# Kernel optimization log

Measured on AMD Instinct MI355X. Metric: run time of the kernel, lower is better.

The kernel has to match this reference:

```python
import jax, jax.numpy as jnp
import numpy as np

Z_WHAT = 64      # z_what latent size
DEC = 64         # decoded object patch size
IMG = 128        # output canvas size (ssd_config.DATA.SHAPE[0])
HID = 1024       # what-decoder hidden size
FEATURE_MAPS = [4, 2, 1]
BOXES_PER_LOC = [2, 2, 2]
B = 16


def build_indices():
    # Faithful port of Decoder.reconstruction_indices
    idx = []
    img_idx = last = 0
    for fm, bpl in zip(FEATURE_MAPS, BOXES_PER_LOC):
        for f in range(fm * fm):
            img_idx = last + f
            idx.append(np.full(bpl, img_idx, dtype=np.int32))
        last = img_idx + 1
    return np.concatenate(idx)


def setup_inputs() -> dict:
    key = jax.random.key(0)
    ks = jax.random.split(key, 6)
    idx = build_indices()
    N = idx.shape[0]            # 42 boxes
    NL = int(idx.max()) + 1     # 21 locations
    z_present = jax.random.randint(ks[4], (B, N, 1), 0, 2, jnp.int32)
    z_present = z_present.at[:, 0, 0].set(1)  # ensure >=1 present per image
    return {
        "z_what": jax.random.normal(ks[0], (B, NL, Z_WHAT), jnp.float32),
        "z_where": jax.random.uniform(ks[1], (B, N, 4), jnp.float32, 0.05, 0.95),
        "z_depth": jax.random.normal(ks[2], (B, NL, 1), jnp.float32),
        "w1": jax.random.normal(ks[3], (Z_WHAT, HID), jnp.float32) * 0.05,
        "b1": jnp.zeros((HID,), jnp.float32),
        "w2": jax.random.normal(ks[5], (HID, 3 * DEC * DEC), jnp.float32) * 0.05,
        "b2": jnp.zeros((3 * DEC * DEC,), jnp.float32),
        "z_present": z_present,
        "indices": jnp.asarray(idx),
    }


def _sample_one(img, px, py):
    # Bilinear grid-sample (zeros padding, align_corners=False) of one
    # [3,S,S] patch at pixel coords px, py of shape [H,W].
    S = img.shape[-1]
    x0 = jnp.floor(px)
    y0 = jnp.floor(py)
    wx = px - x0
    wy = py - y0
    x0i = x0.astype(jnp.int32)
    y0i = y0.astype(jnp.int32)

    def gather(xi, yi):
        valid = (xi >= 0) & (xi < S) & (yi >= 0) & (yi < S)
        v = img[:, jnp.clip(yi, 0, S - 1), jnp.clip(xi, 0, S - 1)]
        return v * valid[None].astype(img.dtype)

    return (gather(x0i, y0i) * ((1 - wx) * (1 - wy))[None]
            + gather(x0i + 1, y0i) * (wx * (1 - wy))[None]
            + gather(x0i, y0i + 1) * ((1 - wx) * wy)[None]
            + gather(x0i + 1, y0i + 1) * (wx * wy)[None])


def _forward(z_what, z_where, z_depth, w1, b1, w2, b2, z_present, indices):
    Bb, NL, D = z_what.shape
    N = indices.shape[0]
    # index_select: expand per-location latents to per-box
    zw = jnp.take(z_what, indices, axis=1)          # [B,N,D]
    zd = jnp.take(z_depth, indices, axis=1)[..., 0]  # [B,N]

    # WhatDecoder: MLP -> sigmoid -> [B*N,3,DEC,DEC] object patches
    h = jax.nn.relu(zw.reshape(-1, D) @ w1 + b1)
    dec = jax.nn.sigmoid(h @ w2 + b2).reshape(-1, 3, DEC, DEC)

    # WhereTransformer: place each patch into IMG x IMG canvas via
    # inverse-affine STN from z_where = (cx, cy, w, h) in [0,1].
    zwf = z_where.reshape(-1, 4)
    cx, cy, w, hh = zwf[:, 0], zwf[:, 1], zwf[:, 2], zwf[:, 3]
    t = (jnp.arange(IMG, dtype=z_what.dtype) + 0.5) / IMG * 2.0 - 1.0
    xt = t[None, :]  # [1,IMG]
    yt = t[:, None]  # [IMG,1]
    xs = (xt[None] - (2 * cx - 1)[:, None, None]) / jnp.maximum(w, 1e-6)[:, None, None]
    ys = (yt[None] - (2 * cy - 1)[:, None, None]) / jnp.maximum(hh, 1e-6)[:, None, None]
    px = ((xs + 1) * DEC - 1) / 2  # [B*N,IMG,IMG]
    py = ((ys + 1) * DEC - 1) / 2
    trans = jax.vmap(_sample_one)(dec, px, py).reshape(Bb, N, 3, IMG, IMG)

    # Masked softmax over depth == padded softmax with -inf starter in the
    # original: absent objects get exactly zero merge weight.
    masked = jnp.where(z_present[..., 0] == 1, zd, -jnp.inf)
    wgt = jax.nn.softmax(masked, axis=1)  # [B,N]
    return jnp.einsum('bn,bnchw->bchw', wgt, trans)


def reference(z_what, z_where, z_depth, w1, b1, w2, b2, z_present, indices):
    return _forward(z_what, z_where, z_depth, w1, b1, w2, b2, z_present, indices)
```

## Files before the change

### kernel.cpp

```cpp
#include <hip/hip_runtime.h>

#define B_    16
#define NL    21
#define NG    42
#define ZW    64
#define HID   1024
#define IMG   128
#define NOUT  12288
#define MROWS 336
#define MPAD  384

typedef __bf16 bf16x8 __attribute__((ext_vector_type(8)));
typedef float f32x4 __attribute__((ext_vector_type(4)));
typedef unsigned short ushort8v __attribute__((ext_vector_type(8)));
typedef unsigned short ushort4v __attribute__((ext_vector_type(4)));

static __device__ __forceinline__ unsigned short f2bf(float f) {
    union { float f; unsigned int u; } v; v.f = f;
    unsigned int r = v.u + 0x7fffu + ((v.u >> 16) & 1u);
    return (unsigned short)(r >> 16);
}

static __device__ __forceinline__ void gload_lds16(const void* g, void* l) {
    __builtin_amdgcn_global_load_lds(
        (const __attribute__((address_space(1))) void*)g,
        (__attribute__((address_space(3))) void*)l,
        16, 0, 0);
}

__global__ __launch_bounds__(256) void k0_w2_transpose(const float* __restrict__ w2,
                                                       unsigned short* __restrict__ w2t) {
    __shared__ float tile[64][65];
    const int nt = blockIdx.x;
    const int kt = blockIdx.y;
    const int t  = threadIdx.x;
    const int n0 = nt * 64, k0 = kt * 64;
    #pragma unroll
    for (int i = 0; i < 4; ++i) {
        int lin = i * 256 + t;
        int kr  = lin >> 4;
        int nc  = (lin & 15) << 2;
        float4 v = *reinterpret_cast<const float4*>(w2 + (size_t)(k0 + kr) * NOUT + n0 + nc);
        tile[kr][nc + 0] = v.x; tile[kr][nc + 1] = v.y;
        tile[kr][nc + 2] = v.z; tile[kr][nc + 3] = v.w;
    }
    __syncthreads();
    #pragma unroll
    for (int i = 0; i < 4; ++i) {
        int lin = i * 256 + t;
        int nc  = lin >> 4;
        int kc  = (lin & 15) << 2;
        ushort4v r;
        r.x = f2bf(tile[kc + 0][nc]);
        r.y = f2bf(tile[kc + 1][nc]);
        r.z = f2bf(tile[kc + 2][nc]);
        r.w = f2bf(tile[kc + 3][nc]);
        int kc_s = kc ^ ((nc & 7) << 3);
        *reinterpret_cast<ushort4v*>(w2t + (size_t)(n0 + nc) * HID + k0 + kc_s) = r;
    }
}

__global__ __launch_bounds__(256) void k1_h(const float* __restrict__ z_what,
                                            const float* __restrict__ w1,
                                            const float* __restrict__ b1,
                                            unsigned short* __restrict__ h) {
    const int r = blockIdx.x, t = threadIdx.x;
    const int sw = (r & 7) << 3;
    if (r >= MROWS) {
        #pragma unroll
        for (int i = 0; i < 4; ++i) {
            int k = t + i * 256;
            h[(size_t)r * HID + ((k & ~63) | ((k & 63) ^ sw))] = 0;
        }
        return;
    }
    __shared__ float zs[ZW];
    if (t < ZW) zs[t] = z_what[(size_t)r * ZW + t];
    __syncthreads();
    float acc[4];
    #pragma unroll
    for (int i = 0; i < 4; ++i) acc[i] = b1[t + i * 256];
    for (int k = 0; k < ZW; ++k) {
        float z = zs[k];
        const float* wr = w1 + (size_t)k * HID + t;
        acc[0] = fmaf(z, wr[0],   acc[0]);
        acc[1] = fmaf(z, wr[256], acc[1]);
        acc[2] = fmaf(z, wr[512], acc[2]);
        acc[3] = fmaf(z, wr[768], acc[3]);
    }
    #pragma unroll
    for (int i = 0; i < 4; ++i) {
        int k = t + i * 256;
        h[(size_t)r * HID + ((k & ~63) | ((k & 63) ^ sw))] =
            f2bf(acc[i] > 0.f ? acc[i] : 0.f);
    }
}

__global__ void k3_params(const float* __restrict__ z_where,
                          const float* __restrict__ z_depth,
                          const int* __restrict__ z_present,
                          const int* __restrict__ indices,
                          float* __restrict__ params) {
    const int b = blockIdx.x, t = threadIdx.x;
    const bool valid = t < NG;
    int idx  = valid ? indices[t] : 0;
    int pres = valid ? z_present[b * NG + t] : 0;
    float zd = z_depth[b * NL + idx];
    const bool on = valid && (pres == 1);
    float val = on ? zd : -__builtin_inff();
    float m = val;
    #pragma unroll
    for (int off = 32; off; off >>= 1) m = fmaxf(m, __shfl_xor(m, off));
    float e = on ? __expf(val - m) : 0.f;
    float s = e;
    #pragma unroll
    for (int off = 32; off; off >>= 1) s += __shfl_xor(s, off);
    if (valid) {
        float wn = e / s;
        const float* zw = z_where + (size_t)(b * NG + t) * 4;
        float cx = zw[0], cy = zw[1], ww = zw[2], hh = zw[3];
        float wm = fmaxf(ww, 1e-6f), hm = fmaxf(hh, 1e-6f);
        float Ax = 32.f / wm, Ay = 32.f / hm;
        float Bx = 31.5f - (2.f * cx - 1.f) * Ax;
        float By = 31.5f - (2.f * cy - 1.f) * Ay;
        float xlof = ((-1.f - Bx) / Ax + 1.f) * 64.f - 0.5f;
        float xhif = (( 64.f - Bx) / Ax + 1.f) * 64.f - 0.5f;
        float ylof = ((-1.f - By) / Ay + 1.f) * 64.f - 0.5f;
        float yhif = (( 64.f - By) / Ay + 1.f) * 64.f - 0.5f;
        int xlo = max(0,   (int)floorf(xlof));
        int xhi = min(128, (int)floorf(xhif) + 2);
        int ylo = max(0,   (int)floorf(ylof));
        int yhi = min(128, (int)floorf(yhif) + 2);
        float* p = params + (size_t)(b * NG + t) * 16;
        p[0] = wn; p[1] = Ax; p[2] = Bx; p[3] = Ay; p[4] = By;
        p[5] = __int_as_float(b * NL + idx);
        p[6] = __int_as_float(xlo); p[7] = __int_as_float(xhi);
        p[8] = __int_as_float(ylo); p[9] = __int_as_float(yhi);
    }
}

__global__ __launch_bounds__(256) void k2_gemm(const unsigned short* __restrict__ h,
                                               const unsigned short* __restrict__ w2t,
                                               const float* __restrict__ b2,
                                               float* __restrict__ dec) {
    __shared__ char smem[65536];
    const int t    = threadIdx.x;
    const int bn   = blockIdx.x;
    const int bm   = blockIdx.y;
    const int row0 = bm * 128, col0 = bn * 128;
    const int lane = t & 63, wid = t >> 6;
    const int wr = (wid >> 1) * 64, wc = (wid & 1) * 64;

    f32x4 acc[4][4];
    const f32x4 zero = {0.f, 0.f, 0.f, 0.f};
    #pragma unroll
    for (int m = 0; m < 4; ++m)
        #pragma unroll
        for (int n = 0; n < 4; ++n) acc[m][n] = zero;

    const char* hB = (const char*)h   + ((size_t)row0 << 11);
    const char* wB = (const char*)w2t + ((size_t)col0 << 11);

    #define STAGE(kt_, buf_)                                                        \
        do {                                                                        \
            int kby = (kt_) << 7;                                    \
            char* ldsA = smem + (buf_) * 32768;                                     \
            char* ldsB = ldsA + 16384;                                              \
            _Pragma("unroll")                                                       \
            for (int r_ = 0; r_ < 4; ++r_) {                                        \
                int ci  = r_ * 256 + t;                                             \
                int row = ci >> 3, kc = ci & 7;                                     \
                gload_lds16(hB + ((size_t)row << 11) + kby + (kc << 4),             \
                            ldsA + ci * 16);                                        \
                gload_lds16(wB + ((size_t)row << 11) + kby + (kc << 4),             \
                            ldsB + ci * 16);                                        \
            }                                                                       \
        } while (0)

    #define COMPUTE(buf_)                                                           \
        do {                                                                        \
            const char* Ab = smem + (buf_) * 32768;                                 \
            const char* Bb = Ab + 16384;                                            \
            _Pragma("unroll")                                                       \
            for (int ks = 0; ks < 2; ++ks) {                                        \
                int kb = ks * 64 + ((lane >> 4) << 4);                              \
                bf16x8 a[4], bb[4];                                                 \
                _Pragma("unroll")                                                   \
                for (int m = 0; m < 4; ++m) {                                       \
                    int row = wr + m * 16 + (lane & 15);                            \
                    a[m] = *reinterpret_cast<const bf16x8*>(                        \
                        Ab + row * 128 + (kb ^ ((row & 7) << 4)));                  \
                }                                                                   \
                _Pragma("unroll")                                                   \
                for (int n = 0; n < 4; ++n) {                                       \
                    int col = wc + n * 16 + (lane & 15);                            \
                    bb[n] = *reinterpret_cast<const bf16x8*>(                       \
                        Bb + col * 128 + (kb ^ ((col & 7) << 4)));                  \
                }                                                                   \
                _Pragma("unroll")                                                   \
                for (int m = 0; m < 4; ++m)                                         \
                    _Pragma("unroll")                                               \
                    for (int n = 0; n < 4; ++n)                                     \
                        acc[m][n] = __builtin_amdgcn_mfma_f32_16x16x32_bf16(        \
                            a[m], bb[n], acc[m][n], 0, 0, 0);                       \
            }                                                                       \
        } while (0)

    STAGE(0, 0);
    __syncthreads();
    int cur = 0;
    for (int kt = 1; kt < 16; ++kt) {
        STAGE(kt, cur ^ 1);
        COMPUTE(cur);
        __syncthreads();
        cur ^= 1;
    }
    COMPUTE(cur);

    const int rbase = row0 + wr + ((lane >> 4) << 2);
    const int cbase = col0 + wc + (lane & 15);
    #pragma unroll
    for (int n = 0; n < 4; ++n) {
        int col = cbase + n * 16;
        float bias = b2[col];
        #pragma unroll
        for (int m = 0; m < 4; ++m) {
            #pragma unroll
            for (int j = 0; j < 4; ++j) {
                int row = rbase + m * 16 + j;
                float v = acc[m][n][j] + bias;
                dec[(size_t)row * NOUT + col] = 1.f / (1.f + __expf(-v));
            }
        }
    }
    #undef STAGE
    #undef COMPUTE
}

__global__ __launch_bounds__(256) void k4_composite(const float* __restrict__ dec,
                                                    const float* __restrict__ params,
                                                    float* __restrict__ out) {
    __shared__ float Pc[NG * 6];
    __shared__ int s_cnt;
    const int b    = blockIdx.x >> 6;
    const int tile = blockIdx.x & 63;
    const int tx0 = (tile & 7) << 4, ty0 = (tile >> 3) << 4;
    const int t    = threadIdx.x;
    if (t < 64) {
        bool pass = false;
        float wn = 0.f, Ax = 0.f, Bx = 0.f, Ay = 0.f, By = 0.f, ridx = 0.f;
        if (t < NG) {
            const float* p = params + (size_t)(b * NG + t) * 16;
            wn = p[0];
            if (wn != 0.f) {
                int xlo = __float_as_int(p[6]), xhi = __float_as_int(p[7]);
                int ylo = __float_as_int(p[8]), yhi = __float_as_int(p[9]);
                if (xlo < tx0 + 16 && xhi > tx0 && ylo < ty0 + 16 && yhi > ty0) {
                    pass = true; Ax = p[1]; Bx = p[2]; Ay = p[3]; By = p[4]; ridx = p[5];
                }
            }
        }
        unsigned long long mask = __ballot(pass);
        if (pass) {
            int slot = __popcll(mask & ((1ull << t) - 1ull));
            float* q = Pc + slot * 6;
            q[0] = wn; q[1] = Ax; q[2] = Bx; q[3] = Ay; q[4] = By; q[5] = ridx;
        }
        if (t == 0) s_cnt = __popcll(mask);
    }
    __syncthreads();
    const int cnt = s_cnt;
    const int x = tx0 + (t & 15);
    const int y = ty0 + (t >> 4);
    const float xt = (x + 0.5f) * (1.f / 64.f) - 1.f;
    const float yt = (y + 0.5f) * (1.f / 64.f) - 1.f;
    float a0 = 0.f, a1 = 0.f, a2 = 0.f;
    for (int i = 0; i < cnt; ++i) {
        const float* q = Pc + i * 6;
        float wn = q[0];
        float px = fmaf(xt, q[1], q[2]);
        float py = fmaf(yt, q[3], q[4]);
        if (!(px > -1.f && px < 64.f && py > -1.f && py < 64.f)) continue;
        float x0f = floorf(px), y0f = floorf(py);
        float wx = px - x0f, wy = py - y0f;
        int x0 = (int)x0f, y0 = (int)y0f;
        int x1 = x0 + 1, y1 = y0 + 1;
        bool vx0 = x0 >= 0, vx1 = x1 < 64, vy0 = y0 >= 0, vy1 = y1 < 64;
        int ridx = __float_as_int(q[5]);
        const float* base = dec + (size_t)ridx * NOUT;
        float w00 = (1.f - wx) * (1.f - wy), w10 = wx * (1.f - wy);
        float w01 = (1.f - wx) * wy,         w11 = wx * wy;
        int o00 = y0 * 64 + x0, o10 = y0 * 64 + x1;
        int o01 = y1 * 64 + x0, o11 = y1 * 64 + x1;
        #pragma unroll
        for (int c = 0; c < 3; ++c) {
            const float* cb = base + c * 4096;
            float v00 = (vx0 && vy0) ? cb[o00] : 0.f;
            float v10 = (vx1 && vy0) ? cb[o10] : 0.f;
            float v01 = (vx0 && vy1) ? cb[o01] : 0.f;
            float v11 = (vx1 && vy1) ? cb[o11] : 0.f;
            float sv = v00 * w00 + v10 * w10 + v01 * w01 + v11 * w11;
            if      (c == 0) a0 = fmaf(wn, sv, a0);
            else if (c == 1) a1 = fmaf(wn, sv, a1);
            else             a2 = fmaf(wn, sv, a2);
        }
    }
    out[((size_t)(b * 3 + 0) * IMG + y) * IMG + x] = a0;
    out[((size_t)(b * 3 + 1) * IMG + y) * IMG + x] = a1;
    out[((size_t)(b * 3 + 2) * IMG + y) * IMG + x] = a2;
}

extern "C" void kernel_launch(void* const* d_in, const int* in_sizes, int n_in,
                              void* d_out, int out_size, void* d_ws, size_t ws_size,
                              hipStream_t stream) {
    const float* z_what   = (const float*)d_in[0];
    const float* z_where  = (const float*)d_in[1];
    const float* z_depth  = (const float*)d_in[2];
    const float* w1       = (const float*)d_in[3];
    const float* b1       = (const float*)d_in[4];
    const float* w2       = (const float*)d_in[5];
    const float* b2       = (const float*)d_in[6];
    const int*   z_present= (const int*)d_in[7];
    const int*   indices  = (const int*)d_in[8];
    float* out = (float*)d_out;

    char* ws = (char*)d_ws;
    unsigned short* w2t = (unsigned short*)ws;
    unsigned short* h   = (unsigned short*)(ws + 25165824);
    float*          dec = (float*)(ws + 25165824 + 786432);
    float*       params = (float*)(ws + 25165824 + 786432 + 18874368);

    hipLaunchKernelGGL(k0_w2_transpose, dim3(192, 16), dim3(256), 0, stream, w2, w2t);
    hipLaunchKernelGGL(k1_h,            dim3(MPAD),    dim3(256), 0, stream, z_what, w1, b1, h);
    hipLaunchKernelGGL(k3_params,       dim3(B_),      dim3(64),  0, stream, z_where, z_depth, z_present, indices, params);
    hipLaunchKernelGGL(k2_gemm,         dim3(96, 3),   dim3(256), 0, stream, h, w2t, b2, dec);
    hipLaunchKernelGGL(k4_composite,    dim3(1024),    dim3(256), 0, stream, dec, params, out);
}
```

Before: 145.3 us.

## Fuse all decoder stages into one cooperative persistent kernel with grid syncs

Replaces the five separate launches (transpose, hidden layer, params, GEMM, composite) with a single cooperative kernel of 256 persistent blocks that loops over tasks per phase and separates phases with grid-wide syncs. If cooperative launch fails, it falls back to three kernels, with the first three stages merged into one launch. The aim is to remove launch overhead and inter-kernel gaps. The cost is grid sync latency and a less even distribution, since the 288 GEMM tiles over 256 blocks create a tail wave.

```diff
diff --git a/kernel.cpp b/kernel.cpp
--- a/kernel.cpp
+++ b/kernel.cpp
@@ -1,4 +1,7 @@
 #include <hip/hip_runtime.h>
+#include <hip/hip_cooperative_groups.h>
+
+namespace cg = cooperative_groups;
 
 #define B_    16
 #define NL    21
@@ -9,10 +12,10 @@
 #define NOUT  12288
 #define MROWS 336
 #define MPAD  384
+#define CGRID 256
 
 typedef __bf16 bf16x8 __attribute__((ext_vector_type(8)));
 typedef float f32x4 __attribute__((ext_vector_type(4)));
-typedef unsigned short ushort8v __attribute__((ext_vector_type(8)));
 typedef unsigned short ushort4v __attribute__((ext_vector_type(4)));
 
 static __device__ __forceinline__ unsigned short f2bf(float f) {
@@ -28,19 +31,20 @@
         16, 0, 0);
 }
 
-__global__ __launch_bounds__(256) void k0_w2_transpose(const float* __restrict__ w2,
-                                                       unsigned short* __restrict__ w2t) {
-    __shared__ float tile[64][65];
-    const int nt = blockIdx.x;
-    const int kt = blockIdx.y;
-    const int t  = threadIdx.x;
-    const int n0 = nt * 64, k0 = kt * 64;
+
+static __device__ __forceinline__ void phaseA_tile(const float* __restrict__ w2,
+                                                   unsigned short* __restrict__ w2t,
+                                                   int task, int t, char* smem) {
+    float (*tile)[65] = reinterpret_cast<float (*)[65]>(smem);
+    const int nt = task % 192, kt = task / 192;
+    const int n0 = nt * 64,    k0 = kt * 64;
     #pragma unroll
     for (int i = 0; i < 4; ++i) {
         int lin = i * 256 + t;
         int kr  = lin >> 4;
         int nc  = (lin & 15) << 2;
-        float4 v = *reinterpret_cast<const float4*>(w2 + (size_t)(k0 + kr) * NOUT + n0 + nc);
+        float4 v = *reinterpret_cast<const float4*>(
+            w2 + (size_t)(k0 + kr) * NOUT + n0 + nc);
         tile[kr][nc + 0] = v.x; tile[kr][nc + 1] = v.y;
         tile[kr][nc + 2] = v.z; tile[kr][nc + 3] = v.w;
     }
@@ -56,15 +60,17 @@
         r.z = f2bf(tile[kc + 2][nc]);
         r.w = f2bf(tile[kc + 3][nc]);
         int kc_s = kc ^ ((nc & 7) << 3);
-        *reinterpret_cast<ushort4v*>(w2t + (size_t)(n0 + nc) * HID + k0 + kc_s) = r;
-    }
-}
-
-__global__ __launch_bounds__(256) void k1_h(const float* __restrict__ z_what,
-                                            const float* __restrict__ w1,
-                                            const float* __restrict__ b1,
-                                            unsigned short* __restrict__ h) {
-    const int r = blockIdx.x, t = threadIdx.x;
+        *reinterpret_cast<ushort4v*>(
+            w2t + (size_t)(n0 + nc) * HID + k0 + kc_s) = r;
+    }
+    __syncthreads();
+}
+
+static __device__ __forceinline__ void phaseB_row(const float* __restrict__ z_what,
+                                                  const float* __restrict__ w1,
+                                                  const float* __restrict__ b1,
+                                                  unsigned short* __restrict__ h,
+                                                  int r, int t, char* smem) {
     const int sw = (r & 7) << 3;
     if (r >= MROWS) {
         #pragma unroll
@@ -74,7 +80,7 @@
         }
         return;
     }
-    __shared__ float zs[ZW];
+    float* zs = reinterpret_cast<float*>(smem);
     if (t < ZW) zs[t] = z_what[(size_t)r * ZW + t];
     __syncthreads();
     float acc[4];
@@ -94,14 +100,16 @@
         h[(size_t)r * HID + ((k & ~63) | ((k & 63) ^ sw))] =
             f2bf(acc[i] > 0.f ? acc[i] : 0.f);
     }
-}
-
-__global__ void k3_params(const float* __restrict__ z_where,
-                          const float* __restrict__ z_depth,
-                          const int* __restrict__ z_present,
-                          const int* __restrict__ indices,
-                          float* __restrict__ params) {
-    const int b = blockIdx.x, t = threadIdx.x;
+    __syncthreads();
+}
+
+static __device__ __forceinline__ void phaseC_batch(const float* __restrict__ z_where,
+                                                    const float* __restrict__ z_depth,
+                                                    const int* __restrict__ z_present,
+                                                    const int* __restrict__ indices,
+                                                    float* __restrict__ params,
+                                                    int b, int t) {
+    if (t >= 64) return;
     const bool valid = t < NG;
     int idx  = valid ? indices[t] : 0;
     int pres = valid ? z_present[b * NG + t] : 0;
@@ -139,14 +147,13 @@
     }
 }
 
-__global__ __launch_bounds__(256) void k2_gemm(const unsigned short* __restrict__ h,
-                                               const unsigned short* __restrict__ w2t,
-                                               const float* __restrict__ b2,
-                                               float* __restrict__ dec) {
-    __shared__ char smem[65536];
-    const int t    = threadIdx.x;
-    const int bn   = blockIdx.x;
-    const int bm   = blockIdx.y;
+static __device__ __forceinline__ void phaseD_tile(const unsigned short* __restrict__ h,
+                                                   const unsigned short* __restrict__ w2t,
+                                                   const float* __restrict__ b2,
+                                                   float* __restrict__ dec,
+                                                   int task, int t, char* smem) {
+    const int bn   = task % 96;
+    const int bm   = task / 96;
     const int row0 = bm * 128, col0 = bn * 128;
     const int lane = t & 63, wid = t >> 6;
     const int wr = (wid >> 1) * 64, wc = (wid & 1) * 64;
@@ -161,49 +168,49 @@
     const char* hB = (const char*)h   + ((size_t)row0 << 11);
     const char* wB = (const char*)w2t + ((size_t)col0 << 11);
 
-    #define STAGE(kt_, buf_)                                                        \
-        do {                                                                        \
-            int kby = (kt_) << 7;                                    \
-            char* ldsA = smem + (buf_) * 32768;                                     \
-            char* ldsB = ldsA + 16384;                                              \
-            _Pragma("unroll")                                                       \
-            for (int r_ = 0; r_ < 4; ++r_) {                                        \
-                int ci  = r_ * 256 + t;                                             \
-                int row = ci >> 3, kc = ci & 7;                                     \
-                gload_lds16(hB + ((size_t)row << 11) + kby + (kc << 4),             \
-                            ldsA + ci * 16);                                        \
-                gload_lds16(wB + ((size_t)row << 11) + kby + (kc << 4),             \
-                            ldsB + ci * 16);                                        \
-            }                                                                       \
+    #define STAGE(kt_, buf_)                                                    \
+        do {                                                                    \
+            int kby = (kt_) << 7;                                               \
+            char* ldsA = smem + (buf_) * 32768;                                 \
+            char* ldsB = ldsA + 16384;                                          \
+            _Pragma("unroll")                                                   \
+            for (int r_ = 0; r_ < 4; ++r_) {                                    \
+                int ci  = r_ * 256 + t;                                         \
+                int row = ci >> 3, kc = ci & 7;                                 \
+                gload_lds16(hB + ((size_t)row << 11) + kby + (kc << 4),         \
+                            ldsA + ci * 16);                                    \
+                gload_lds16(wB + ((size_t)row << 11) + kby + (kc << 4),         \
+                            ldsB + ci * 16);                                    \
+            }                                                                   \
         } while (0)
 
-    #define COMPUTE(buf_)                                                           \
-        do {                                                                        \
-            const char* Ab = smem + (buf_) * 32768;                                 \
-            const char* Bb = Ab + 16384;                                            \
-            _Pragma("unroll")                                                       \
-            for (int ks = 0; ks < 2; ++ks) {                                        \
-                int kb = ks * 64 + ((lane >> 4) << 4);                              \
-                bf16x8 a[4], bb[4];                                                 \
-                _Pragma("unroll")                                                   \
-                for (int m = 0; m < 4; ++m) {                                       \
-                    int row = wr + m * 16 + (lane & 15);                            \
-                    a[m] = *reinterpret_cast<const bf16x8*>(                        \
-                        Ab + row * 128 + (kb ^ ((row & 7) << 4)));                  \
-                }                                                                   \
-                _Pragma("unroll")                                                   \
-                for (int n = 0; n < 4; ++n) {                                       \
-                    int col = wc + n * 16 + (lane & 15);                            \
-                    bb[n] = *reinterpret_cast<const bf16x8*>(                       \
-                        Bb + col * 128 + (kb ^ ((col & 7) << 4)));                  \
-                }                                                                   \
-                _Pragma("unroll")                                                   \
-                for (int m = 0; m < 4; ++m)                                         \
-                    _Pragma("unroll")                                               \
-                    for (int n = 0; n < 4; ++n)                                     \
-                        acc[m][n] = __builtin_amdgcn_mfma_f32_16x16x32_bf16(        \
-                            a[m], bb[n], acc[m][n], 0, 0, 0);                       \
-            }                                                                       \
+    #define COMPUTE(buf_)                                                       \
+        do {                                                                    \
+            const char* Ab = smem + (buf_) * 32768;                             \
+            const char* Bb = Ab + 16384;                                        \
+            _Pragma("unroll")                                                   \
+            for (int ks = 0; ks < 2; ++ks) {                                    \
+                int kb = ks * 64 + ((lane >> 4) << 4);                          \
+                bf16x8 a[4], bb[4];                                             \
+                _Pragma("unroll")                                               \
+                for (int m = 0; m < 4; ++m) {                                   \
+                    int row = wr + m * 16 + (lane & 15);                        \
+                    a[m] = *reinterpret_cast<const bf16x8*>(                    \
+                        Ab + row * 128 + (kb ^ ((row & 7) << 4)));              \
+                }                                                               \
+                _Pragma("unroll")                                               \
+                for (int n = 0; n < 4; ++n) {                                   \
+                    int col = wc + n * 16 + (lane & 15);                        \
+                    bb[n] = *reinterpret_cast<const bf16x8*>(                   \
+                        Bb + col * 128 + (kb ^ ((col & 7) << 4)));              \
+                }                                                               \
+                _Pragma("unroll")                                               \
+                for (int m = 0; m < 4; ++m)                                     \
+                    _Pragma("unroll")                                           \
+                    for (int n = 0; n < 4; ++n)                                 \
+                        acc[m][n] = __builtin_amdgcn_mfma_f32_16x16x32_bf16(    \
+                            a[m], bb[n], acc[m][n], 0, 0, 0);                   \
+            }                                                                   \
         } while (0)
 
     STAGE(0, 0);
@@ -216,6 +223,8 @@
         cur ^= 1;
     }
     COMPUTE(cur);
+    #undef STAGE
+    #undef COMPUTE
 
     const int rbase = row0 + wr + ((lane >> 4) << 2);
     const int cbase = col0 + wc + (lane & 15);
@@ -233,19 +242,18 @@
             }
         }
     }
-    #undef STAGE
-    #undef COMPUTE
-}
-
-__global__ __launch_bounds__(256) void k4_composite(const float* __restrict__ dec,
-                                                    const float* __restrict__ params,
-                                                    float* __restrict__ out) {
-    __shared__ float Pc[NG * 6];
-    __shared__ int s_cnt;
-    const int b    = blockIdx.x >> 6;
-    const int tile = blockIdx.x & 63;
+    __syncthreads();
+}
+
+static __device__ __forceinline__ void phaseE_tile(const float* __restrict__ dec,
+                                                   const float* __restrict__ params,
+                                                   float* __restrict__ out,
+                                                   int task, int t, char* smem) {
+    float* Pc    = reinterpret_cast<float*>(smem);
+    int*   s_cnt = reinterpret_cast<int*>(smem + NG * 6 * 4);
+    const int b    = task >> 6;
+    const int tile = task & 63;
     const int tx0 = (tile & 7) << 4, ty0 = (tile >> 3) << 4;
-    const int t    = threadIdx.x;
     if (t < 64) {
         bool pass = false;
         float wn = 0.f, Ax = 0.f, Bx = 0.f, Ay = 0.f, By = 0.f, ridx = 0.f;
@@ -266,10 +274,10 @@
             float* q = Pc + slot * 6;
             q[0] = wn; q[1] = Ax; q[2] = Bx; q[3] = Ay; q[4] = By; q[5] = ridx;
         }
-        if (t == 0) s_cnt = __popcll(mask);
-    }
-    __syncthreads();
-    const int cnt = s_cnt;
+        if (t == 0) *s_cnt = __popcll(mask);
+    }
+    __syncthreads();
+    const int cnt = *s_cnt;
     const int x = tx0 + (t & 15);
     const int y = ty0 + (t >> 4);
     const float xt = (x + 0.5f) * (1.f / 64.f) - 1.f;
@@ -308,20 +316,85 @@
     out[((size_t)(b * 3 + 0) * IMG + y) * IMG + x] = a0;
     out[((size_t)(b * 3 + 1) * IMG + y) * IMG + x] = a1;
     out[((size_t)(b * 3 + 2) * IMG + y) * IMG + x] = a2;
+    __syncthreads();
+}
+
+__global__ __launch_bounds__(256, 2) void fused_decoder(
+    const float* __restrict__ z_what,  const float* __restrict__ z_where,
+    const float* __restrict__ z_depth, const float* __restrict__ w1,
+    const float* __restrict__ b1,      const float* __restrict__ w2,
+    const float* __restrict__ b2,      const int* __restrict__ z_present,
+    const int* __restrict__ indices,
+    unsigned short* __restrict__ w2t,  unsigned short* __restrict__ h,
+    float* __restrict__ dec,           float* __restrict__ params,
+    float* __restrict__ out)
+{
+    __shared__ char smem[65536];
+    cg::grid_group grid = cg::this_grid();
+    const int bx = blockIdx.x;
+    const int t  = threadIdx.x;
+
+    for (int task = bx; task < 3072; task += CGRID) phaseA_tile(w2, w2t, task, t, smem);
+    for (int r    = bx; r    < MPAD; r    += CGRID) phaseB_row(z_what, w1, b1, h, r, t, smem);
+    if (bx < B_) phaseC_batch(z_where, z_depth, z_present, indices, params, bx, t);
+
+    __threadfence();
+    grid.sync();
+    __threadfence();
+
+    for (int task = bx; task < 288; task += CGRID) phaseD_tile(h, w2t, b2, dec, task, t, smem);
+
+    __threadfence();
+    grid.sync();
+    __threadfence();
+
+    for (int task = bx; task < 1024; task += CGRID) phaseE_tile(dec, params, out, task, t, smem);
+}
+
+__global__ __launch_bounds__(256) void kABC(
+    const float* __restrict__ z_what, const float* __restrict__ z_where,
+    const float* __restrict__ z_depth, const float* __restrict__ w1,
+    const float* __restrict__ b1, const float* __restrict__ w2,
+    const int* __restrict__ z_present, const int* __restrict__ indices,
+    unsigned short* __restrict__ w2t, unsigned short* __restrict__ h,
+    float* __restrict__ params)
+{
+    __shared__ char smem[16640];
+    const int bx = blockIdx.x, t = threadIdx.x;
+    if (bx < 3072)      phaseA_tile(w2, w2t, bx, t, smem);
+    else if (bx < 3456) phaseB_row(z_what, w1, b1, h, bx - 3072, t, smem);
+    else                phaseC_batch(z_where, z_depth, z_present, indices, params, bx - 3456, t);
+}
+
+__global__ __launch_bounds__(256) void kD(const unsigned short* __restrict__ h,
+                                          const unsigned short* __restrict__ w2t,
+                                          const float* __restrict__ b2,
+                                          float* __restrict__ dec)
+{
+    __shared__ char smem[65536];
+    phaseD_tile(h, w2t, b2, dec, blockIdx.x, threadIdx.x, smem);
+}
+
+__global__ __launch_bounds__(256) void kE(const float* __restrict__ dec,
+                                          const float* __restrict__ params,
+                                          float* __restrict__ out)
+{
+    __shared__ char smem[2048];
+    phaseE_tile(dec, params, out, blockIdx.x, threadIdx.x, smem);
 }
 
 extern "C" void kernel_launch(void* const* d_in, const int* in_sizes, int n_in,
                               void* d_out, int out_size, void* d_ws, size_t ws_size,
                               hipStream_t stream) {
-    const float* z_what   = (const float*)d_in[0];
-    const float* z_where  = (const float*)d_in[1];
-    const float* z_depth  = (const float*)d_in[2];
-    const float* w1       = (const float*)d_in[3];
-    const float* b1       = (const float*)d_in[4];
-    const float* w2       = (const float*)d_in[5];
-    const float* b2       = (const float*)d_in[6];
-    const int*   z_present= (const int*)d_in[7];
-    const int*   indices  = (const int*)d_in[8];
+    const float* z_what    = (const float*)d_in[0];
+    const float* z_where   = (const float*)d_in[1];
+    const float* z_depth   = (const float*)d_in[2];
+    const float* w1        = (const float*)d_in[3];
+    const float* b1        = (const float*)d_in[4];
+    const float* w2        = (const float*)d_in[5];
+    const float* b2        = (const float*)d_in[6];
+    const int*   z_present = (const int*)d_in[7];
+    const int*   indices   = (const int*)d_in[8];
     float* out = (float*)d_out;
 
     char* ws = (char*)d_ws;
@@ -330,9 +403,20 @@
     float*          dec = (float*)(ws + 25165824 + 786432);
     float*       params = (float*)(ws + 25165824 + 786432 + 18874368);
 
-    hipLaunchKernelGGL(k0_w2_transpose, dim3(192, 16), dim3(256), 0, stream, w2, w2t);
-    hipLaunchKernelGGL(k1_h,            dim3(MPAD),    dim3(256), 0, stream, z_what, w1, b1, h);
-    hipLaunchKernelGGL(k3_params,       dim3(B_),      dim3(64),  0, stream, z_where, z_depth, z_present, indices, params);
-    hipLaunchKernelGGL(k2_gemm,         dim3(96, 3),   dim3(256), 0, stream, h, w2t, b2, dec);
-    hipLaunchKernelGGL(k4_composite,    dim3(1024),    dim3(256), 0, stream, dec, params, out);
-}
+    void* args[] = {
+        (void*)&z_what, (void*)&z_where, (void*)&z_depth, (void*)&w1, (void*)&b1,
+        (void*)&w2, (void*)&b2, (void*)&z_present, (void*)&indices,
+        (void*)&w2t, (void*)&h, (void*)&dec, (void*)&params, (void*)&out
+    };
+    hipError_t err = hipLaunchCooperativeKernel((const void*)fused_decoder,
+                                                dim3(CGRID), dim3(256),
+                                                args, 0, stream);
+    if (err != hipSuccess) {
+        (void)hipGetLastError();
+        hipLaunchKernelGGL(kABC, dim3(3472), dim3(256), 0, stream,
+                           z_what, z_where, z_depth, w1, b1, w2,
+                           z_present, indices, w2t, h, params);
+        hipLaunchKernelGGL(kD, dim3(288), dim3(256), 0, stream, h, w2t, b2, dec);
+        hipLaunchKernelGGL(kE, dim3(1024), dim3(256), 0, stream, dec, params, out);
+    }
+}
```

New measurement: 466.2 us. 221% more time.
